# Kernel tuning notes

Hardware: AMD Instinct MI355X
Metric: run time of the kernel (lower is better)

Reference implementation:

```python
import jax, jax.numpy as jnp
import numpy as np

# dims: batch B, frames F_, spatial tokens N, heads H, head dim D, model dim DIM
B, F_, N, H, D, DIM = 1, 16, 1024, 8, 64, 512


def setup_inputs() -> dict:
    key = jax.random.key(0)
    k1, k2, k3, k4 = jax.random.split(key, 4)
    x = jax.random.normal(k1, (B, F_ * N, DIM), dtype=jnp.float32)
    W_qkv = jax.random.normal(k2, (DIM, 3 * H * D), dtype=jnp.float32) * 0.02
    W_out = jax.random.normal(k3, (H * D, DIM), dtype=jnp.float32) * 0.02
    mask = jax.random.randint(k4, (1, 1, N), 0, 2, dtype=jnp.int32)
    return {"x": x, "W_qkv": W_qkv, "W_out": W_out, "mask": mask, "diag": 1}


def reference(x, W_qkv, W_out, mask, diag):
    scale = D ** -0.5
    qkv = x @ W_qkv                      # [B, F*N, 3*H*D]
    q, k, v = jnp.split(qkv, 3, axis=-1)

    def split_heads(t):                  # 'b n (h d) -> (b h) n d'
        return t.reshape(B, F_ * N, H, D).transpose(0, 2, 1, 3).reshape(B * H, F_ * N, D)

    q, k, v = map(split_heads, (q, k, v))
    q = q * scale

    def axial(t):                        # '(b h) (f n) d -> (b h f) n d'
        return t.reshape(B * H * F_, N, D)

    q, k, v = map(axial, (q, k, v))

    sim = jnp.einsum('bid,bjd->bij', q, k)        # [(B*H*F), N, N]
    neg = -jnp.finfo(sim.dtype).max
    if diag:
        sim = jnp.where(jnp.eye(N, dtype=bool)[None], neg, sim)
    sim = jnp.where(mask == 0, neg, sim)           # padding mask broadcast
    attn = jax.nn.softmax(sim, axis=-1)
    out = jnp.einsum('bij,bjd->bid', attn, v)      # [(B*H*F), N, D]

    # '(b h f) n d -> (b h) (f n) d' then '(b h) n d -> b n (h d)'
    out = out.reshape(B, H, F_ * N, D).transpose(0, 2, 1, 3).reshape(B, F_ * N, H * D)
    return out @ W_out
```

## Files before the change

### kernel.cpp

```cpp
#include <hip/hip_runtime.h>
#include <stdint.h>

typedef __bf16 bf16;
typedef __bf16 bf16x8 __attribute__((ext_vector_type(8)));
typedef float f32x4 __attribute__((ext_vector_type(4)));

__device__ __forceinline__ void gload_lds16(const void* g, void* l) {
    __builtin_amdgcn_global_load_lds((const __attribute__((address_space(1))) void*)g,
                                     (__attribute__((address_space(3))) void*)l, 16, 0, 0);
}

__device__ __forceinline__ float fast_exp2(float x) { return __builtin_amdgcn_exp2f(x); }

__global__ __launch_bounds__(256) void k_prep(const float* __restrict__ x, bf16* __restrict__ xb,
                                              const float* __restrict__ Wqkv, bf16* __restrict__ WqT,
                                              const float* __restrict__ Wout, bf16* __restrict__ WoT,
                                              const int* __restrict__ mask, int* __restrict__ idxU,
                                              int* __restrict__ cpos, int* __restrict__ meta) {
    __shared__ float t[32][33];
    __shared__ int lsum[256];
    int b = blockIdx.x, tid = threadIdx.x;
    if (b < 4096) {
        int i = b * 256 + tid;
        const f32x4* p = (const f32x4*)(x + (size_t)i * 8);
        f32x4 a = p[0], c = p[1];
        bf16x8 o;
        o[0] = (bf16)a[0]; o[1] = (bf16)a[1]; o[2] = (bf16)a[2]; o[3] = (bf16)a[3];
        o[4] = (bf16)c[0]; o[5] = (bf16)c[1]; o[6] = (bf16)c[2]; o[7] = (bf16)c[3];
        *(bf16x8*)(xb + (size_t)i * 8) = o;
    } else if (b < 4096 + 768 + 256) {
        const float* W; bf16* WT; int C, bb;
        if (b < 4096 + 768) { W = Wqkv; WT = WqT; C = 1536; bb = b - 4096; }
        else                { W = Wout; WT = WoT; C = 512;  bb = b - 4864; }
        int nblk = C / 32;
        int n0 = (bb % nblk) * 32, k0 = (bb / nblk) * 32;
        int tx = tid & 31, ty = tid >> 5;
        for (int i = 0; i < 32; i += 8) t[ty + i][tx] = W[(size_t)(k0 + ty + i) * C + n0 + tx];
        __syncthreads();
        for (int i = 0; i < 32; i += 8) WT[(size_t)(n0 + ty + i) * 512 + k0 + tx] = (bf16)t[tx][ty + i];
    } else {
        int m[4], s = 0;
#pragma unroll
        for (int e = 0; e < 4; e++) { m[e] = mask[4 * tid + e]; s += m[e]; }
        lsum[tid] = s;
        __syncthreads();
        for (int off = 1; off < 256; off <<= 1) {
            int v = (tid >= off) ? lsum[tid - off] : 0;
            __syncthreads();
            lsum[tid] += v;
            __syncthreads();
        }
        int run = lsum[tid] - s;
#pragma unroll
        for (int e = 0; e < 4; e++) {
            if (m[e]) { idxU[run] = 4 * tid + e; cpos[4 * tid + e] = run; run++; }
            else cpos[4 * tid + e] = -1;
        }
        int nU = lsum[255];
        for (int i = nU + tid; i < 1024; i += 256) idxU[i] = 0;
        if (tid == 255) { meta[0] = nU; meta[1] = (nU + 63) >> 6; }
    }
}

__global__ __launch_bounds__(256) void k_qkv(const bf16* __restrict__ Xb, const bf16* __restrict__ WT,
                                             bf16* __restrict__ Qb, bf16* __restrict__ Kb, bf16* __restrict__ Vb) {
    __shared__ char As[2][8192], Bs[2][8192];
    int tid = threadIdx.x, l = tid & 63, w = tid >> 6;
    int wy = w >> 1, wx = w & 1;
    int id = blockIdx.x;
    int wg = (id & 7) * 192 + (id >> 3);
    int bm = (wg / 12) * 128, bn = (wg % 12) * 128;
    int lr = l & 15, kg = l >> 4;

    int subr = l >> 2, chk = l & 3;
    int R0 = w * 32 + subr,     m0 = (R0 >> 1) & 3, c0 = chk ^ m0;
    int R1 = w * 32 + 16 + subr, m1 = (R1 >> 1) & 3, c1 = chk ^ m1;

    f32x4 acc[4][4] = {};

    gload_lds16((const char*)Xb + ((size_t)(bm + R0) * 512) * 2 + c0 * 16, As[0] + w * 2048 + l * 16);
    gload_lds16((const char*)Xb + ((size_t)(bm + R1) * 512) * 2 + c1 * 16, As[0] + w * 2048 + 1024 + l * 16);
    gload_lds16((const char*)WT + ((size_t)(bn + R0) * 512) * 2 + c0 * 16, Bs[0] + w * 2048 + l * 16);
    gload_lds16((const char*)WT + ((size_t)(bn + R1) * 512) * 2 + c1 * 16, Bs[0] + w * 2048 + 1024 + l * 16);
    __syncthreads();

    for (int t = 0; t < 16; t++) {
        int cur = t & 1;
        if (t < 15) {
            int k1 = (t + 1) * 32;
            gload_lds16((const char*)Xb + ((size_t)(bm + R0) * 512 + k1) * 2 + c0 * 16, As[cur ^ 1] + w * 2048 + l * 16);
            gload_lds16((const char*)Xb + ((size_t)(bm + R1) * 512 + k1) * 2 + c1 * 16, As[cur ^ 1] + w * 2048 + 1024 + l * 16);
            gload_lds16((const char*)WT + ((size_t)(bn + R0) * 512 + k1) * 2 + c0 * 16, Bs[cur ^ 1] + w * 2048 + l * 16);
            gload_lds16((const char*)WT + ((size_t)(bn + R1) * 512 + k1) * 2 + c1 * 16, Bs[cur ^ 1] + w * 2048 + 1024 + l * 16);
        }

        bf16x8 af[4], bfr[4];
#pragma unroll
        for (int mt = 0; mt < 4; mt++) {
            int r = wy * 64 + mt * 16 + lr;
            af[mt] = *(const bf16x8*)(As[cur] + r * 64 + ((kg ^ ((r >> 1) & 3)) << 4));
        }
#pragma unroll
        for (int nt = 0; nt < 4; nt++) {
            int r = wx * 64 + nt * 16 + lr;
            bfr[nt] = *(const bf16x8*)(Bs[cur] + r * 64 + ((kg ^ ((r >> 1) & 3)) << 4));
        }
#pragma unroll
        for (int mt = 0; mt < 4; mt++)
#pragma unroll
            for (int nt = 0; nt < 4; nt++)
                acc[mt][nt] = __builtin_amdgcn_mfma_f32_16x16x32_bf16(af[mt], bfr[nt], acc[mt][nt], 0, 0, 0);

        __syncthreads();
    }

#pragma unroll
    for (int mt = 0; mt < 4; mt++) {
#pragma unroll
        for (int nt = 0; nt < 4; nt++) {
            int c = bn + wx * 64 + nt * 16 + lr;
            int which = c >> 9, hd = c & 511, h = hd >> 6, d = hd & 63;
            float qs = (which == 0) ? 0.18033688f : 1.0f;
            bf16* base = (which == 0) ? Qb : (which == 1) ? Kb : Vb;
#pragma unroll
            for (int j = 0; j < 4; j++) {
                int m = bm + wy * 64 + mt * 16 + kg * 4 + j;
                int f = m >> 10, nn = m & 1023;
                base[((size_t)(h * 16 + f) * 1024 + nn) * 64 + d] = (bf16)(acc[mt][nt][j] * qs);
            }
        }
    }
}

__global__ __launch_bounds__(256) void k_vtg(const bf16* __restrict__ V, bf16* __restrict__ Vtc,
                                             const int* __restrict__ idxU, const int* __restrict__ meta) {
    __shared__ bf16 t[64][80];
    int bp = blockIdx.y, c0 = blockIdx.x * 64;
    int nU = meta[0], nUp = meta[1] << 6;
    if (c0 >= nUp) return;
    int tid = threadIdx.x;
    int nl = tid >> 2, dc = (tid & 3) * 16;
    int c = c0 + nl;
    bf16x8 a0 = {}, a1 = {};
    if (c < nU) {
        int row = idxU[c];
        const bf16* src = V + ((size_t)bp * 1024 + row) * 64 + dc;
        a0 = *(const bf16x8*)src;
        a1 = *(const bf16x8*)(src + 8);
    }
    *(bf16x8*)&t[nl][dc] = a0;
    *(bf16x8*)&t[nl][dc + 8] = a1;
    __syncthreads();
    int dl = tid >> 2, nc = (tid & 3) * 16;
    bf16x8 o0, o1;
#pragma unroll
    for (int i = 0; i < 8; i++) o0[i] = t[nc + i][dl];
#pragma unroll
    for (int i = 0; i < 8; i++) o1[i] = t[nc + 8 + i][dl];
    bf16* dst = Vtc + ((size_t)bp * 64 + dl) * 1024 + c0 + nc;
    *(bf16x8*)dst = o0;
    *(bf16x8*)(dst + 8) = o1;
}

__global__ __launch_bounds__(512) void k_attn(const bf16* __restrict__ Qb, const bf16* __restrict__ Kb,
                                              const bf16* __restrict__ Vtc, bf16* __restrict__ AO,
                                              const int* __restrict__ cpos, const int* __restrict__ idxU,
                                              const int* __restrict__ meta, const int* __restrict__ diagp) {
    __shared__ char Ks[8192], Vs[8192], Ps[16384];
    int tid = threadIdx.x, l = tid & 63, w = tid >> 6;
    int id = blockIdx.x;
    int wg = (id & 7) * 128 + (id >> 3);
    int qt = wg & 7, bp = wg >> 3;
    int lr = l & 15, kg = l >> 4;
    int diag = diagp[0];
    int nU = meta[0], nT = meta[1];

    int nq = qt * 128 + w * 16 + lr;
    const char* Qrow = (const char*)Qb + ((size_t)bp * 1024 + nq) * 128;
    bf16x8 qf0 = *(const bf16x8*)(Qrow + kg * 16);
    bf16x8 qf1 = *(const bf16x8*)(Qrow + 64 + kg * 16);

    int cq[4];
#pragma unroll
    for (int j = 0; j < 4; j++) {
        int qg = qt * 128 + w * 16 + kg * 4 + j;
        cq[j] = diag ? cpos[qg] : -1;
    }

    const char* Kbb = (const char*)Kb + (size_t)bp * 1024 * 128;
    const char* Vbase = (const char*)Vtc + (size_t)bp * 64 * 2048;

    int rs = tid >> 3;
    int cs = (tid & 7) ^ (rs & 7);

    f32x4 o[4] = {};
    f32x4 psum = {0.f, 0.f, 0.f, 0.f};

    for (int kt = 0; kt < nT; kt++) {
        __syncthreads();
        int krow = idxU[kt * 64 + rs];
        gload_lds16(Kbb + (size_t)krow * 128 + cs * 16, Ks + w * 1024);
        gload_lds16(Vbase + (size_t)rs * 2048 + kt * 128 + cs * 16, Vs + w * 1024);
        __syncthreads();

        f32x4 s[4] = {};
        __builtin_amdgcn_s_setprio(1);
#pragma unroll
        for (int nt = 0; nt < 4; nt++) {
            int r = nt * 16 + lr;
            bf16x8 kf0 = *(const bf16x8*)(Ks + r * 128 + ((kg ^ (r & 7)) << 4));
            bf16x8 kf1 = *(const bf16x8*)(Ks + r * 128 + (((4 + kg) ^ (r & 7)) << 4));
            s[nt] = __builtin_amdgcn_mfma_f32_16x16x32_bf16(qf0, kf0, s[nt], 0, 0, 0);
            s[nt] = __builtin_amdgcn_mfma_f32_16x16x32_bf16(qf1, kf1, s[nt], 0, 0, 0);
        }
        __builtin_amdgcn_s_setprio(0);

        float mf0 = (kt * 64 + lr < nU) ? 1.f : 0.f;
        float mf1 = (kt * 64 + 16 + lr < nU) ? 1.f : 0.f;
        float mf2 = (kt * 64 + 32 + lr < nU) ? 1.f : 0.f;
        float mf3 = (kt * 64 + 48 + lr < nU) ? 1.f : 0.f;
#pragma unroll
        for (int j = 0; j < 4; j++) {
            s[0][j] = fast_exp2(s[0][j]) * mf0;
            s[1][j] = fast_exp2(s[1][j]) * mf1;
            s[2][j] = fast_exp2(s[2][j]) * mf2;
            s[3][j] = fast_exp2(s[3][j]) * mf3;
        }
#pragma unroll
        for (int nt = 0; nt < 4; nt++) {
            int c = kt * 64 + nt * 16 + lr;
#pragma unroll
            for (int j = 0; j < 4; j++)
                if (c == cq[j]) s[nt][j] = 0.f;
        }
#pragma unroll
        for (int j = 0; j < 4; j++) psum[j] += (s[0][j] + s[1][j]) + (s[2][j] + s[3][j]);

#pragma unroll
        for (int nt = 0; nt < 4; nt++)
#pragma unroll
            for (int j = 0; j < 4; j++) {
                int rq = w * 16 + kg * 4 + j;
                int byte = (rq * 128 + (nt * 16 + lr) * 2) ^ ((rq & 7) << 4);
                *(bf16*)(Ps + byte) = (bf16)s[nt][j];
            }

        int rp = w * 16 + lr;
        bf16x8 pf0 = *(const bf16x8*)(Ps + rp * 128 + ((kg ^ (rp & 7)) << 4));
        bf16x8 pf1 = *(const bf16x8*)(Ps + rp * 128 + (((4 + kg) ^ (rp & 7)) << 4));
        __builtin_amdgcn_s_setprio(1);
#pragma unroll
        for (int dt = 0; dt < 4; dt++) {
            int rd = dt * 16 + lr;
            bf16x8 vf0 = *(const bf16x8*)(Vs + rd * 128 + ((kg ^ (rd & 7)) << 4));
            bf16x8 vf1 = *(const bf16x8*)(Vs + rd * 128 + (((4 + kg) ^ (rd & 7)) << 4));
            o[dt] = __builtin_amdgcn_mfma_f32_16x16x32_bf16(pf0, vf0, o[dt], 0, 0, 0);
            o[dt] = __builtin_amdgcn_mfma_f32_16x16x32_bf16(pf1, vf1, o[dt], 0, 0, 0);
        }
        __builtin_amdgcn_s_setprio(0);
    }

#pragma unroll
    for (int off = 1; off < 16; off <<= 1)
#pragma unroll
        for (int j = 0; j < 4; j++) psum[j] += __shfl_xor(psum[j], off, 64);
    float inv[4];
#pragma unroll
    for (int j = 0; j < 4; j++) inv[j] = 1.0f / psum[j];

    int f = bp & 15, h = bp >> 4;
#pragma unroll
    for (int dt = 0; dt < 4; dt++)
#pragma unroll
        for (int j = 0; j < 4; j++) {
            int n = qt * 128 + w * 16 + kg * 4 + j;
            size_t m = (size_t)f * 1024 + n;
            AO[m * 512 + h * 64 + dt * 16 + lr] = (bf16)(o[dt][j] * inv[j]);
        }
}

__global__ __launch_bounds__(256) void k_out(const bf16* __restrict__ Ab, const bf16* __restrict__ WT,
                                             float* __restrict__ out) {
    __shared__ char As[16384], Bs[16384];
    int tid = threadIdx.x, l = tid & 63, w = tid >> 6;
    int wy = w >> 1, wx = w & 1;
    int id = blockIdx.x;
    int wg = (id & 7) * 64 + (id >> 3);
    int bm = (wg / 4) * 128, bn = (wg % 4) * 128;
    int lr = l & 15, kg = l >> 4;
    int p = l & 7, rsub = l >> 3;
    int csrc = p ^ rsub;
    f32x4 acc[4][4] = {};

    for (int k0 = 0; k0 < 512; k0 += 64) {
        __syncthreads();
#pragma unroll
        for (int i = 0; i < 4; i++) {
            int rt = w * 32 + i * 8 + rsub;
            gload_lds16((const char*)Ab + ((size_t)(bm + rt) * 512 + k0) * 2 + csrc * 16,
                        As + w * 4096 + i * 1024 + l * 16);
            gload_lds16((const char*)WT + ((size_t)(bn + rt) * 512 + k0) * 2 + csrc * 16,
                        Bs + w * 4096 + i * 1024 + l * 16);
        }
        __syncthreads();
#pragma unroll
        for (int kk = 0; kk < 2; kk++) {
            bf16x8 af[4], bfr[4];
            int sb = (kk * 4 + kg);
#pragma unroll
            for (int mt = 0; mt < 4; mt++) {
                int r = wy * 64 + mt * 16 + lr;
                af[mt] = *(const bf16x8*)(As + r * 128 + ((sb ^ (lr & 7)) << 4));
            }
#pragma unroll
            for (int nt = 0; nt < 4; nt++) {
                int r = wx * 64 + nt * 16 + lr;
                bfr[nt] = *(const bf16x8*)(Bs + r * 128 + ((sb ^ (lr & 7)) << 4));
            }
#pragma unroll
            for (int mt = 0; mt < 4; mt++)
#pragma unroll
                for (int nt = 0; nt < 4; nt++)
                    acc[mt][nt] = __builtin_amdgcn_mfma_f32_16x16x32_bf16(af[mt], bfr[nt], acc[mt][nt], 0, 0, 0);
        }
    }
#pragma unroll
    for (int mt = 0; mt < 4; mt++)
#pragma unroll
        for (int nt = 0; nt < 4; nt++) {
            int c = bn + wx * 64 + nt * 16 + lr;
#pragma unroll
            for (int j = 0; j < 4; j++) {
                int m = bm + wy * 64 + mt * 16 + kg * 4 + j;
                out[(size_t)m * 512 + c] = acc[mt][nt][j];
            }
        }
}

extern "C" void kernel_launch(void* const* d_in, const int* in_sizes, int n_in,
                              void* d_out, int out_size, void* d_ws, size_t ws_size,
                              hipStream_t stream) {
    const float* x    = (const float*)d_in[0];
    const float* Wqkv = (const float*)d_in[1];
    const float* Wout = (const float*)d_in[2];
    const int*   mask = (const int*)d_in[3];
    const int*   diag = (const int*)d_in[4];
    float* out = (float*)d_out;
    char* ws = (char*)d_ws;

    bf16* Xb  = (bf16*)(ws);
    bf16* Vtc = (bf16*)(ws);
    bf16* WqT = (bf16*)(ws + ((size_t)16 << 20));
    bf16* WoT = (bf16*)(ws + ((size_t)18 << 20));
    int*  idxU = (int*)(ws + ((size_t)18 << 20) + (1 << 19));
    int*  cpos = (int*)(ws + ((size_t)18 << 20) + (1 << 19) + 4096);
    int*  meta = (int*)(ws + ((size_t)18 << 20) + (1 << 19) + 8192);
    bf16* Qb  = (bf16*)(ws + ((size_t)19 << 20));
    bf16* Kb  = (bf16*)(ws + ((size_t)35 << 20));
    bf16* Vb  = (bf16*)(ws + ((size_t)51 << 20));
    bf16* AO  = (bf16*)(ws + ((size_t)67 << 20));

    hipLaunchKernelGGL(k_prep, dim3(4096 + 768 + 256 + 1), dim3(256), 0, stream,
                       x, Xb, Wqkv, WqT, Wout, WoT, mask, idxU, cpos, meta);
    hipLaunchKernelGGL(k_qkv, dim3(1536), dim3(256), 0, stream, Xb, WqT, Qb, Kb, Vb);
    hipLaunchKernelGGL(k_vtg, dim3(16, 128), dim3(256), 0, stream, Vb, Vtc, idxU, meta);
    hipLaunchKernelGGL(k_attn, dim3(1024), dim3(512), 0, stream, Qb, Kb, Vtc, AO, cpos, idxU, meta, diag);
    hipLaunchKernelGGL(k_out, dim3(512), dim3(256), 0, stream, AO, WoT, out);
}
```

Baseline: 110.3 us.

## Double-buffer K/V tiles in attention and A/B tiles in output GEMM

The attention kernel drops its single 64-key tile for double-buffered 32-key tiles. Half the waves stage K and half stage V, so the next tile's global-to-LDS load overlaps the current tile's MFMAs, and each step needs one barrier instead of two. The padding-mask multiply is now applied only on the last partial tile, and the diagonal check is simplified. The output projection GEMM is restructured the same way, using double-buffered 32-wide k-steps like the QKV kernel. The cost is more loop iterations with smaller MFMA batches per barrier, plus an unpadded P buffer with an 80-byte row stride that may cause LDS bank conflicts.

```diff
diff --git a/kernel.cpp b/kernel.cpp
--- a/kernel.cpp
+++ b/kernel.cpp
@@ -73,7 +73,7 @@
     int lr = l & 15, kg = l >> 4;
 
     int subr = l >> 2, chk = l & 3;
-    int R0 = w * 32 + subr,     m0 = (R0 >> 1) & 3, c0 = chk ^ m0;
+    int R0 = w * 32 + subr,      m0 = (R0 >> 1) & 3, c0 = chk ^ m0;
     int R1 = w * 32 + 16 + subr, m1 = (R1 >> 1) & 3, c1 = chk ^ m1;
 
     f32x4 acc[4][4] = {};
@@ -166,7 +166,7 @@
                                               const bf16* __restrict__ Vtc, bf16* __restrict__ AO,
                                               const int* __restrict__ cpos, const int* __restrict__ idxU,
                                               const int* __restrict__ meta, const int* __restrict__ diagp) {
-    __shared__ char Ks[8192], Vs[8192], Ps[16384];
+    __shared__ char Ks[2][4096], Vs[2][4096], Ps[10240];
     int tid = threadIdx.x, l = tid & 63, w = tid >> 6;
     int id = blockIdx.x;
     int wg = (id & 7) * 128 + (id >> 3);
@@ -174,6 +174,7 @@
     int lr = l & 15, kg = l >> 4;
     int diag = diagp[0];
     int nU = meta[0], nT = meta[1];
+    int nsteps = nT * 2;
 
     int nq = qt * 128 + w * 16 + lr;
     const char* Qrow = (const char*)Qb + ((size_t)bp * 1024 + nq) * 128;
@@ -190,74 +191,88 @@
     const char* Kbb = (const char*)Kb + (size_t)bp * 1024 * 128;
     const char* Vbase = (const char*)Vtc + (size_t)bp * 64 * 2048;
 
-    int rs = tid >> 3;
-    int cs = (tid & 7) ^ (rs & 7);
+    bool stK = (w < 4);
+    int sw = w & 3;
+    int k_lrow = sw * 8 + (l >> 3);
+    int k_cs = (l & 7) ^ (l >> 3);
+    int v_row = sw * 16 + (l >> 2);
+    int v_cs = (l & 3) ^ ((v_row >> 1) & 3);
 
     f32x4 o[4] = {};
     f32x4 psum = {0.f, 0.f, 0.f, 0.f};
 
-    for (int kt = 0; kt < nT; kt++) {
-        __syncthreads();
-        int krow = idxU[kt * 64 + rs];
-        gload_lds16(Kbb + (size_t)krow * 128 + cs * 16, Ks + w * 1024);
-        gload_lds16(Vbase + (size_t)rs * 2048 + kt * 128 + cs * 16, Vs + w * 1024);
-        __syncthreads();
-
-        f32x4 s[4] = {};
+    if (stK) {
+        int krow = idxU[k_lrow];
+        gload_lds16(Kbb + (size_t)krow * 128 + k_cs * 16, Ks[0] + sw * 1024);
+    } else {
+        gload_lds16(Vbase + (size_t)v_row * 2048 + v_cs * 16, Vs[0] + sw * 1024);
+    }
+    __syncthreads();
+
+    for (int t = 0; t < nsteps; t++) {
+        int cur = t & 1;
+        if (t + 1 < nsteps) {
+            if (stK) {
+                int krow = idxU[(t + 1) * 32 + k_lrow];
+                gload_lds16(Kbb + (size_t)krow * 128 + k_cs * 16, Ks[cur ^ 1] + sw * 1024);
+            } else {
+                gload_lds16(Vbase + (size_t)v_row * 2048 + (t + 1) * 64 + v_cs * 16, Vs[cur ^ 1] + sw * 1024);
+            }
+        }
+
+        f32x4 s[2] = {};
         __builtin_amdgcn_s_setprio(1);
 #pragma unroll
-        for (int nt = 0; nt < 4; nt++) {
+        for (int nt = 0; nt < 2; nt++) {
             int r = nt * 16 + lr;
-            bf16x8 kf0 = *(const bf16x8*)(Ks + r * 128 + ((kg ^ (r & 7)) << 4));
-            bf16x8 kf1 = *(const bf16x8*)(Ks + r * 128 + (((4 + kg) ^ (r & 7)) << 4));
+            bf16x8 kf0 = *(const bf16x8*)(Ks[cur] + r * 128 + ((kg ^ (r & 7)) << 4));
+            bf16x8 kf1 = *(const bf16x8*)(Ks[cur] + r * 128 + (((4 + kg) ^ (r & 7)) << 4));
             s[nt] = __builtin_amdgcn_mfma_f32_16x16x32_bf16(qf0, kf0, s[nt], 0, 0, 0);
             s[nt] = __builtin_amdgcn_mfma_f32_16x16x32_bf16(qf1, kf1, s[nt], 0, 0, 0);
         }
         __builtin_amdgcn_s_setprio(0);
 
-        float mf0 = (kt * 64 + lr < nU) ? 1.f : 0.f;
-        float mf1 = (kt * 64 + 16 + lr < nU) ? 1.f : 0.f;
-        float mf2 = (kt * 64 + 32 + lr < nU) ? 1.f : 0.f;
-        float mf3 = (kt * 64 + 48 + lr < nU) ? 1.f : 0.f;
 #pragma unroll
         for (int j = 0; j < 4; j++) {
-            s[0][j] = fast_exp2(s[0][j]) * mf0;
-            s[1][j] = fast_exp2(s[1][j]) * mf1;
-            s[2][j] = fast_exp2(s[2][j]) * mf2;
-            s[3][j] = fast_exp2(s[3][j]) * mf3;
-        }
-#pragma unroll
-        for (int nt = 0; nt < 4; nt++) {
-            int c = kt * 64 + nt * 16 + lr;
-#pragma unroll
-            for (int j = 0; j < 4; j++)
-                if (c == cq[j]) s[nt][j] = 0.f;
-        }
-#pragma unroll
-        for (int j = 0; j < 4; j++) psum[j] += (s[0][j] + s[1][j]) + (s[2][j] + s[3][j]);
-
-#pragma unroll
-        for (int nt = 0; nt < 4; nt++)
+            s[0][j] = fast_exp2(s[0][j]);
+            s[1][j] = fast_exp2(s[1][j]);
+        }
+        if (t * 32 + 32 > nU) {
+            float mf0 = (t * 32 + lr < nU) ? 1.f : 0.f;
+            float mf1 = (t * 32 + 16 + lr < nU) ? 1.f : 0.f;
+#pragma unroll
+            for (int j = 0; j < 4; j++) { s[0][j] *= mf0; s[1][j] *= mf1; }
+        }
+#pragma unroll
+        for (int j = 0; j < 4; j++) {
+            if ((cq[j] >> 5) == t) {
+                int ntd = (cq[j] >> 4) & 1;
+                if ((cq[j] & 15) == lr) s[ntd][j] = 0.f;
+            }
+        }
+#pragma unroll
+        for (int j = 0; j < 4; j++) psum[j] += s[0][j] + s[1][j];
+
+#pragma unroll
+        for (int nt = 0; nt < 2; nt++)
 #pragma unroll
             for (int j = 0; j < 4; j++) {
                 int rq = w * 16 + kg * 4 + j;
-                int byte = (rq * 128 + (nt * 16 + lr) * 2) ^ ((rq & 7) << 4);
-                *(bf16*)(Ps + byte) = (bf16)s[nt][j];
+                *(bf16*)(Ps + rq * 80 + (nt * 16 + lr) * 2) = (bf16)s[nt][j];
             }
 
         int rp = w * 16 + lr;
-        bf16x8 pf0 = *(const bf16x8*)(Ps + rp * 128 + ((kg ^ (rp & 7)) << 4));
-        bf16x8 pf1 = *(const bf16x8*)(Ps + rp * 128 + (((4 + kg) ^ (rp & 7)) << 4));
+        bf16x8 pf = *(const bf16x8*)(Ps + rp * 80 + kg * 16);
         __builtin_amdgcn_s_setprio(1);
 #pragma unroll
         for (int dt = 0; dt < 4; dt++) {
             int rd = dt * 16 + lr;
-            bf16x8 vf0 = *(const bf16x8*)(Vs + rd * 128 + ((kg ^ (rd & 7)) << 4));
-            bf16x8 vf1 = *(const bf16x8*)(Vs + rd * 128 + (((4 + kg) ^ (rd & 7)) << 4));
-            o[dt] = __builtin_amdgcn_mfma_f32_16x16x32_bf16(pf0, vf0, o[dt], 0, 0, 0);
-            o[dt] = __builtin_amdgcn_mfma_f32_16x16x32_bf16(pf1, vf1, o[dt], 0, 0, 0);
+            bf16x8 vf = *(const bf16x8*)(Vs[cur] + rd * 64 + ((kg ^ ((rd >> 1) & 3)) << 4));
+            o[dt] = __builtin_amdgcn_mfma_f32_16x16x32_bf16(pf, vf, o[dt], 0, 0, 0);
         }
         __builtin_amdgcn_s_setprio(0);
+
+        __syncthreads();
     }
 
 #pragma unroll
@@ -281,49 +296,56 @@
 
 __global__ __launch_bounds__(256) void k_out(const bf16* __restrict__ Ab, const bf16* __restrict__ WT,
                                              float* __restrict__ out) {
-    __shared__ char As[16384], Bs[16384];
+    __shared__ char As[2][8192], Bs[2][8192];
     int tid = threadIdx.x, l = tid & 63, w = tid >> 6;
     int wy = w >> 1, wx = w & 1;
     int id = blockIdx.x;
     int wg = (id & 7) * 64 + (id >> 3);
     int bm = (wg / 4) * 128, bn = (wg % 4) * 128;
     int lr = l & 15, kg = l >> 4;
-    int p = l & 7, rsub = l >> 3;
-    int csrc = p ^ rsub;
+
+    int subr = l >> 2, chk = l & 3;
+    int R0 = w * 32 + subr,      m0 = (R0 >> 1) & 3, c0 = chk ^ m0;
+    int R1 = w * 32 + 16 + subr, m1 = (R1 >> 1) & 3, c1 = chk ^ m1;
+
     f32x4 acc[4][4] = {};
 
-    for (int k0 = 0; k0 < 512; k0 += 64) {
-        __syncthreads();
-#pragma unroll
-        for (int i = 0; i < 4; i++) {
-            int rt = w * 32 + i * 8 + rsub;
-            gload_lds16((const char*)Ab + ((size_t)(bm + rt) * 512 + k0) * 2 + csrc * 16,
-                        As + w * 4096 + i * 1024 + l * 16);
-            gload_lds16((const char*)WT + ((size_t)(bn + rt) * 512 + k0) * 2 + csrc * 16,
-                        Bs + w * 4096 + i * 1024 + l * 16);
-        }
-        __syncthreads();
-#pragma unroll
-        for (int kk = 0; kk < 2; kk++) {
-            bf16x8 af[4], bfr[4];
-            int sb = (kk * 4 + kg);
-#pragma unroll
-            for (int mt = 0; mt < 4; mt++) {
-                int r = wy * 64 + mt * 16 + lr;
-                af[mt] = *(const bf16x8*)(As + r * 128 + ((sb ^ (lr & 7)) << 4));
-            }
-#pragma unroll
-            for (int nt = 0; nt < 4; nt++) {
-                int r = wx * 64 + nt * 16 + lr;
-                bfr[nt] = *(const bf16x8*)(Bs + r * 128 + ((sb ^ (lr & 7)) << 4));
-            }
-#pragma unroll
-            for (int mt = 0; mt < 4; mt++)
-#pragma unroll
-                for (int nt = 0; nt < 4; nt++)
-                    acc[mt][nt] = __builtin_amdgcn_mfma_f32_16x16x32_bf16(af[mt], bfr[nt], acc[mt][nt], 0, 0, 0);
-        }
-    }
+    gload_lds16((const char*)Ab + ((size_t)(bm + R0) * 512) * 2 + c0 * 16, As[0] + w * 2048 + l * 16);
+    gload_lds16((const char*)Ab + ((size_t)(bm + R1) * 512) * 2 + c1 * 16, As[0] + w * 2048 + 1024 + l * 16);
+    gload_lds16((const char*)WT + ((size_t)(bn + R0) * 512) * 2 + c0 * 16, Bs[0] + w * 2048 + l * 16);
+    gload_lds16((const char*)WT + ((size_t)(bn + R1) * 512) * 2 + c1 * 16, Bs[0] + w * 2048 + 1024 + l * 16);
+    __syncthreads();
+
+    for (int t = 0; t < 16; t++) {
+        int cur = t & 1;
+        if (t < 15) {
+            int k1 = (t + 1) * 32;
+            gload_lds16((const char*)Ab + ((size_t)(bm + R0) * 512 + k1) * 2 + c0 * 16, As[cur ^ 1] + w * 2048 + l * 16);
+            gload_lds16((const char*)Ab + ((size_t)(bm + R1) * 512 + k1) * 2 + c1 * 16, As[cur ^ 1] + w * 2048 + 1024 + l * 16);
+            gload_lds16((const char*)WT + ((size_t)(bn + R0) * 512 + k1) * 2 + c0 * 16, Bs[cur ^ 1] + w * 2048 + l * 16);
+            gload_lds16((const char*)WT + ((size_t)(bn + R1) * 512 + k1) * 2 + c1 * 16, Bs[cur ^ 1] + w * 2048 + 1024 + l * 16);
+        }
+
+        bf16x8 af[4], bfr[4];
+#pragma unroll
+        for (int mt = 0; mt < 4; mt++) {
+            int r = wy * 64 + mt * 16 + lr;
+            af[mt] = *(const bf16x8*)(As[cur] + r * 64 + ((kg ^ ((r >> 1) & 3)) << 4));
+        }
+#pragma unroll
+        for (int nt = 0; nt < 4; nt++) {
+            int r = wx * 64 + nt * 16 + lr;
+            bfr[nt] = *(const bf16x8*)(Bs[cur] + r * 64 + ((kg ^ ((r >> 1) & 3)) << 4));
+        }
+#pragma unroll
+        for (int mt = 0; mt < 4; mt++)
+#pragma unroll
+            for (int nt = 0; nt < 4; nt++)
+                acc[mt][nt] = __builtin_amdgcn_mfma_f32_16x16x32_bf16(af[mt], bfr[nt], acc[mt][nt], 0, 0, 0);
+
+        __syncthreads();
+    }
+
 #pragma unroll
     for (int mt = 0; mt < 4; mt++)
 #pragma unroll
```

New measurement: 114.8 us. 4.0% more time.

## Load V fragments directly to registers and double-buffer output GEMM

Applied to the files above, without the earlier changes.

In the attention kernel, V tiles are now read straight from global memory into registers in MFMA fragment layout instead of being staged through LDS. This drops one LDS buffer and its reads. The output projection kernel is restructured into a K=32 double-buffered pipeline, copying the qkv GEMM scheme, so the next tile's loads overlap the current tile's MFMAs. The risks are that the uncoalesced per-lane global V loads may stall the inner loop, and that the smaller K step doubles the number of barriers.

```diff
diff --git a/kernel.cpp b/kernel.cpp
--- a/kernel.cpp
+++ b/kernel.cpp
@@ -73,7 +73,7 @@
     int lr = l & 15, kg = l >> 4;
 
     int subr = l >> 2, chk = l & 3;
-    int R0 = w * 32 + subr,     m0 = (R0 >> 1) & 3, c0 = chk ^ m0;
+    int R0 = w * 32 + subr,      m0 = (R0 >> 1) & 3, c0 = chk ^ m0;
     int R1 = w * 32 + 16 + subr, m1 = (R1 >> 1) & 3, c1 = chk ^ m1;
 
     f32x4 acc[4][4] = {};
@@ -166,7 +166,7 @@
                                               const bf16* __restrict__ Vtc, bf16* __restrict__ AO,
                                               const int* __restrict__ cpos, const int* __restrict__ idxU,
                                               const int* __restrict__ meta, const int* __restrict__ diagp) {
-    __shared__ char Ks[8192], Vs[8192], Ps[16384];
+    __shared__ char Ks[8192], Ps[16384];
     int tid = threadIdx.x, l = tid & 63, w = tid >> 6;
     int id = blockIdx.x;
     int wg = (id & 7) * 128 + (id >> 3);
@@ -189,6 +189,9 @@
 
     const char* Kbb = (const char*)Kb + (size_t)bp * 1024 * 128;
     const char* Vbase = (const char*)Vtc + (size_t)bp * 64 * 2048;
+    const char* Vrow[4];
+#pragma unroll
+    for (int dt = 0; dt < 4; dt++) Vrow[dt] = Vbase + (size_t)(dt * 16 + lr) * 2048 + kg * 16;
 
     int rs = tid >> 3;
     int cs = (tid & 7) ^ (rs & 7);
@@ -200,7 +203,12 @@
         __syncthreads();
         int krow = idxU[kt * 64 + rs];
         gload_lds16(Kbb + (size_t)krow * 128 + cs * 16, Ks + w * 1024);
-        gload_lds16(Vbase + (size_t)rs * 2048 + kt * 128 + cs * 16, Vs + w * 1024);
+        bf16x8 vf[4][2];
+#pragma unroll
+        for (int dt = 0; dt < 4; dt++) {
+            vf[dt][0] = *(const bf16x8*)(Vrow[dt] + kt * 128);
+            vf[dt][1] = *(const bf16x8*)(Vrow[dt] + kt * 128 + 64);
+        }
         __syncthreads();
 
         f32x4 s[4] = {};
@@ -251,11 +259,8 @@
         __builtin_amdgcn_s_setprio(1);
 #pragma unroll
         for (int dt = 0; dt < 4; dt++) {
-            int rd = dt * 16 + lr;
-            bf16x8 vf0 = *(const bf16x8*)(Vs + rd * 128 + ((kg ^ (rd & 7)) << 4));
-            bf16x8 vf1 = *(const bf16x8*)(Vs + rd * 128 + (((4 + kg) ^ (rd & 7)) << 4));
-            o[dt] = __builtin_amdgcn_mfma_f32_16x16x32_bf16(pf0, vf0, o[dt], 0, 0, 0);
-            o[dt] = __builtin_amdgcn_mfma_f32_16x16x32_bf16(pf1, vf1, o[dt], 0, 0, 0);
+            o[dt] = __builtin_amdgcn_mfma_f32_16x16x32_bf16(pf0, vf[dt][0], o[dt], 0, 0, 0);
+            o[dt] = __builtin_amdgcn_mfma_f32_16x16x32_bf16(pf1, vf[dt][1], o[dt], 0, 0, 0);
         }
         __builtin_amdgcn_s_setprio(0);
     }
@@ -281,49 +286,56 @@
 
 __global__ __launch_bounds__(256) void k_out(const bf16* __restrict__ Ab, const bf16* __restrict__ WT,
                                              float* __restrict__ out) {
-    __shared__ char As[16384], Bs[16384];
+    __shared__ char As[2][8192], Bs[2][8192];
     int tid = threadIdx.x, l = tid & 63, w = tid >> 6;
     int wy = w >> 1, wx = w & 1;
     int id = blockIdx.x;
     int wg = (id & 7) * 64 + (id >> 3);
     int bm = (wg / 4) * 128, bn = (wg % 4) * 128;
     int lr = l & 15, kg = l >> 4;
-    int p = l & 7, rsub = l >> 3;
-    int csrc = p ^ rsub;
+
+    int subr = l >> 2, chk = l & 3;
+    int R0 = w * 32 + subr,      m0 = (R0 >> 1) & 3, c0 = chk ^ m0;
+    int R1 = w * 32 + 16 + subr, m1 = (R1 >> 1) & 3, c1 = chk ^ m1;
+
     f32x4 acc[4][4] = {};
 
-    for (int k0 = 0; k0 < 512; k0 += 64) {
-        __syncthreads();
-#pragma unroll
-        for (int i = 0; i < 4; i++) {
-            int rt = w * 32 + i * 8 + rsub;
-            gload_lds16((const char*)Ab + ((size_t)(bm + rt) * 512 + k0) * 2 + csrc * 16,
-                        As + w * 4096 + i * 1024 + l * 16);
-            gload_lds16((const char*)WT + ((size_t)(bn + rt) * 512 + k0) * 2 + csrc * 16,
-                        Bs + w * 4096 + i * 1024 + l * 16);
-        }
-        __syncthreads();
-#pragma unroll
-        for (int kk = 0; kk < 2; kk++) {
-            bf16x8 af[4], bfr[4];
-            int sb = (kk * 4 + kg);
-#pragma unroll
-            for (int mt = 0; mt < 4; mt++) {
-                int r = wy * 64 + mt * 16 + lr;
-                af[mt] = *(const bf16x8*)(As + r * 128 + ((sb ^ (lr & 7)) << 4));
-            }
-#pragma unroll
-            for (int nt = 0; nt < 4; nt++) {
-                int r = wx * 64 + nt * 16 + lr;
-                bfr[nt] = *(const bf16x8*)(Bs + r * 128 + ((sb ^ (lr & 7)) << 4));
-            }
-#pragma unroll
-            for (int mt = 0; mt < 4; mt++)
-#pragma unroll
-                for (int nt = 0; nt < 4; nt++)
-                    acc[mt][nt] = __builtin_amdgcn_mfma_f32_16x16x32_bf16(af[mt], bfr[nt], acc[mt][nt], 0, 0, 0);
-        }
-    }
+    gload_lds16((const char*)Ab + ((size_t)(bm + R0) * 512) * 2 + c0 * 16, As[0] + w * 2048 + l * 16);
+    gload_lds16((const char*)Ab + ((size_t)(bm + R1) * 512) * 2 + c1 * 16, As[0] + w * 2048 + 1024 + l * 16);
+    gload_lds16((const char*)WT + ((size_t)(bn + R0) * 512) * 2 + c0 * 16, Bs[0] + w * 2048 + l * 16);
+    gload_lds16((const char*)WT + ((size_t)(bn + R1) * 512) * 2 + c1 * 16, Bs[0] + w * 2048 + 1024 + l * 16);
+    __syncthreads();
+
+    for (int t = 0; t < 16; t++) {
+        int cur = t & 1;
+        if (t < 15) {
+            int k1 = (t + 1) * 32;
+            gload_lds16((const char*)Ab + ((size_t)(bm + R0) * 512 + k1) * 2 + c0 * 16, As[cur ^ 1] + w * 2048 + l * 16);
+            gload_lds16((const char*)Ab + ((size_t)(bm + R1) * 512 + k1) * 2 + c1 * 16, As[cur ^ 1] + w * 2048 + 1024 + l * 16);
+            gload_lds16((const char*)WT + ((size_t)(bn + R0) * 512 + k1) * 2 + c0 * 16, Bs[cur ^ 1] + w * 2048 + l * 16);
+            gload_lds16((const char*)WT + ((size_t)(bn + R1) * 512 + k1) * 2 + c1 * 16, Bs[cur ^ 1] + w * 2048 + 1024 + l * 16);
+        }
+
+        bf16x8 af[4], bfr[4];
+#pragma unroll
+        for (int mt = 0; mt < 4; mt++) {
+            int r = wy * 64 + mt * 16 + lr;
+            af[mt] = *(const bf16x8*)(As[cur] + r * 64 + ((kg ^ ((r >> 1) & 3)) << 4));
+        }
+#pragma unroll
+        for (int nt = 0; nt < 4; nt++) {
+            int r = wx * 64 + nt * 16 + lr;
+            bfr[nt] = *(const bf16x8*)(Bs[cur] + r * 64 + ((kg ^ ((r >> 1) & 3)) << 4));
+        }
+#pragma unroll
+        for (int mt = 0; mt < 4; mt++)
+#pragma unroll
+            for (int nt = 0; nt < 4; nt++)
+                acc[mt][nt] = __builtin_amdgcn_mfma_f32_16x16x32_bf16(af[mt], bfr[nt], acc[mt][nt], 0, 0, 0);
+
+        __syncthreads();
+    }
+
 #pragma unroll
     for (int mt = 0; mt < 4; mt++)
 #pragma unroll
```

Measured after the change: 181.0 us. +64.1%, slower.
